# Performance work log

Hardware: AMD Instinct MI355X
Metric: run time of the kernel (lower is better)

The kernel has to match this reference:

```python
import jax, jax.numpy as jnp
import numpy as np

NUM_EXPERTS = 8
EMBED_DIM = 1024
EXPERT_DIM = 2048
TOP_K = 2
B, T = 2, 1024


def setup_inputs() -> dict:
    key = jax.random.key(0)
    ks = jax.random.split(key, 7)
    std = 0.02
    return {
        "x": jax.random.normal(ks[0], (B, T, EMBED_DIM), dtype=jnp.float32),
        "gate_inputs": jax.random.normal(ks[1], (B, T, EMBED_DIM), dtype=jnp.float32),
        "gate_kernel": jax.random.normal(ks[2], (EMBED_DIM, NUM_EXPERTS), dtype=jnp.float32) * std,
        "per_expert_scale": jnp.ones((NUM_EXPERTS,), dtype=jnp.float32),
        "gate_proj_w": jax.random.normal(ks[3], (NUM_EXPERTS, EMBED_DIM, EXPERT_DIM), dtype=jnp.float32) * std,
        "up_proj_w": jax.random.normal(ks[4], (NUM_EXPERTS, EMBED_DIM, EXPERT_DIM), dtype=jnp.float32) * std,
        "down_proj_w": jax.random.normal(ks[5], (NUM_EXPERTS, EXPERT_DIM, EMBED_DIM), dtype=jnp.float32) * std,
    }


def reference(x, gate_inputs, gate_kernel, per_expert_scale,
              gate_proj_w, up_proj_w, down_proj_w):
    Bb, Tt, D = x.shape
    x_flat = x.reshape(Bb * Tt, D)          # [t, e]
    g_flat = gate_inputs.reshape(Bb * Tt, D)

    logits = jnp.dot(g_flat, gate_kernel)   # [t, n]
    topk_logits, topk_idx = jax.lax.top_k(logits, TOP_K)  # [t, k]
    weights = jax.nn.sigmoid(topk_logits)   # [t, k]

    # Dense all-expert projections (as in the original module)
    gate_out = jnp.einsum('te,ned->tnd', x_flat, gate_proj_w)  # [t, n, d]
    up_out = jnp.einsum('te,ned->tnd', x_flat, up_proj_w)
    act = jax.nn.gelu(gate_out) * up_out
    expert_out = jnp.einsum('tnd,nde->tne', act, down_proj_w)  # [t, n, e]
    expert_out = expert_out * per_expert_scale[None, :, None]

    mask = jax.nn.one_hot(topk_idx, NUM_EXPERTS, dtype=expert_out.dtype)  # [t, k, n]
    selected = jnp.einsum('tkn,tne->tke', mask, expert_out)               # [t, k, e]
    out = jnp.einsum('tk,tke->te', weights, selected)                     # [t, e]
    return out.reshape(Bb, Tt, D)
```

## Files before the change

### kernel.cpp

```cpp
#include <hip/hip_runtime.h>
#include <math.h>
#include <stdint.h>

#define NE 8
#define ED 1024
#define FD 2048
#define NTOK 2048
#define BM 128
#define BN 128
#define BK 64

typedef unsigned short u16;
typedef unsigned int u32;
typedef __attribute__((ext_vector_type(4))) float f32x4;
typedef __attribute__((ext_vector_type(8))) short s16x8;
typedef __attribute__((ext_vector_type(4))) unsigned int u32v4;


__device__ __forceinline__ u16 f2bf(float f) {
    u32 u = __builtin_bit_cast(u32, f);
    u32 r = u + 0x7fffu + ((u >> 16) & 1u);
    return (u16)(r >> 16);
}

typedef __attribute__((address_space(1))) const void gvoid_t;
typedef __attribute__((address_space(3))) void lvoid_t;

__device__ __forceinline__ void gload16(const void* g, void* l) {
    __builtin_amdgcn_global_load_lds((gvoid_t*)g, (lvoid_t*)l, 16, 0, 0);
}

#define WS_CNT 0u
#define WS_OFF 64u
#define WS_TOK 256u
#define WS_WT  65792u
#define WS_XB  131328u
#define WS_WG  (8u << 20)
#define WS_WU  41943040u
#define WS_WD  75497472u
#define WS_ACT 109051904u
#define WS_NEED 130023424u


__global__ __launch_bounds__(256) void k_router(
        const float* __restrict__ gin, const float* __restrict__ gk,
        int* __restrict__ cnt, int* __restrict__ tok, float* __restrict__ wl) {
    int lane = threadIdx.x & 63;
    int t = (blockIdx.x * 256 + threadIdx.x) >> 6;
    if (t >= NTOK) return;
    const float* row = gin + (size_t)t * ED;
    float acc[NE];
#pragma unroll
    for (int e = 0; e < NE; e++) acc[e] = 0.f;
    for (int i = lane; i < ED; i += 64) {
        float v = row[i];
        const float* g = gk + i * NE;
#pragma unroll
        for (int e = 0; e < NE; e++) acc[e] = fmaf(v, g[e], acc[e]);
    }
#pragma unroll
    for (int e = 0; e < NE; e++) {
#pragma unroll
        for (int off = 32; off > 0; off >>= 1)
            acc[e] += __shfl_down(acc[e], off, 64);
    }
    if (lane == 0) {
        int b0 = 0; float v0 = acc[0];
#pragma unroll
        for (int e = 1; e < NE; e++) if (acc[e] > v0) { v0 = acc[e]; b0 = e; }
        int b1 = -1; float v1 = -3.4e38f;
#pragma unroll
        for (int e = 0; e < NE; e++) if (e != b0 && acc[e] > v1) { v1 = acc[e]; b1 = e; }
        float w0 = 1.f / (1.f + __expf(-v0));
        float w1 = 1.f / (1.f + __expf(-v1));
        int p0 = atomicAdd(&cnt[b0], 1);
        tok[b0 * NTOK + p0] = t; wl[b0 * NTOK + p0] = w0;
        int p1 = atomicAdd(&cnt[b1], 1);
        tok[b1 * NTOK + p1] = t; wl[b1 * NTOK + p1] = w1;
    }
}

__global__ void k_scan(const int* __restrict__ cnt, int* __restrict__ off) {
    if (threadIdx.x == 0 && blockIdx.x == 0) {
        int a = 0;
#pragma unroll
        for (int e = 0; e < NE; e++) { off[e] = a; a += (cnt[e] + 127) & ~127; }
        off[NE] = a;
    }
}


__global__ __launch_bounds__(256) void k_cvtx(const float4* __restrict__ x, uint2* __restrict__ xb) {
    int i = blockIdx.x * 256 + threadIdx.x;
    float4 v = x[i];
    uint2 o;
    o.x = (u32)f2bf(v.x) | ((u32)f2bf(v.y) << 16);
    o.y = (u32)f2bf(v.z) | ((u32)f2bf(v.w) << 16);
    xb[i] = o;
}


__global__ __launch_bounds__(256) void k_cvtw(
        const float* __restrict__ wgf, const float* __restrict__ wuf, const float* __restrict__ wdf,
        u16* __restrict__ og, u16* __restrict__ ou, u16* __restrict__ od) {
    int b = blockIdx.x;
    const float* src; u16* dst; int NT, KC, ROW;
    if (b < 2048)      { src = wgf; dst = og; NT = 16; KC = 16; ROW = FD; }
    else if (b < 4096) { b -= 2048; src = wuf; dst = ou; NT = 16; KC = 16; ROW = FD; }
    else               { b -= 4096; src = wdf; dst = od; NT = 8;  KC = 32; ROW = ED; }
    int kc = b % KC; int r = b / KC; int nt = r % NT; int e = r / NT;
    const float* base = src + (size_t)e * (size_t)(KC * 64) * ROW + (size_t)kc * 64 * ROW + nt * 128;
    u16* ob = dst + (size_t)b * 8192;

    int tid = threadIdx.x;
    int k0 = (tid & 7) * 8;
    int n0 = tid >> 3;
#pragma unroll
    for (int g4 = 0; g4 < 4; g4++) {
        int n = n0 + 32 * g4;
        const float* p = base + n;
        u32 w[4];
#pragma unroll
        for (int j = 0; j < 4; j++) {
            float a = p[(size_t)(k0 + 2 * j) * ROW];
            float c = p[(size_t)(k0 + 2 * j + 1) * ROW];
            w[j] = (u32)f2bf(a) | ((u32)f2bf(c) << 16);
        }
        *(u32v4*)(ob + (size_t)n * 64 + k0) = (u32v4){w[0], w[1], w[2], w[3]};
    }
}


__global__ __launch_bounds__(256, 2) void k_passA(
        const u16* __restrict__ xb, const u16* __restrict__ wg, const u16* __restrict__ wu,
        const int* __restrict__ cnt, const int* __restrict__ off,
        const int* __restrict__ tok, u16* __restrict__ act) {
    int e = blockIdx.z, mt = blockIdx.y, nt = blockIdx.x;
    int c = cnt[e];
    if (mt * BM >= c) return;
    int rmax = c - mt * BM; if (rmax > BM) rmax = BM;

    __shared__ u16 sA[BM * BK];
    __shared__ u16 sBg[BN * BK];
    __shared__ u16 sBu[BN * BK];

    int tid = threadIdx.x;
    int lane = tid & 63, wv = tid >> 6;
    int wm = wv >> 1, wn = wv & 1;
    int col = lane & 15, quad = lane >> 4;

    f32x4 zero = {0.f, 0.f, 0.f, 0.f};
    f32x4 ag[4][4], au[4][4];
#pragma unroll
    for (int i = 0; i < 4; i++)
#pragma unroll
        for (int j = 0; j < 4; j++) { ag[i][j] = zero; au[i][j] = zero; }

    int am = tid >> 1, ah = tid & 1;
    int ridx = mt * BM + am; if (ridx > c - 1) ridx = c - 1;
    int trow = tok[e * NTOK + ridx];
    const u16* asrc = xb + (size_t)trow * ED + ah * 32;
    u16* adst = sA + am * BK + ah * 32;

    const u16* gg = wg + ((size_t)(e * 16 + nt) * 16) * 8192;
    const u16* gu = wu + ((size_t)(e * 16 + nt) * 16) * 8192;
    const u16* bsrc0 = (wv < 2 ? gg : gu);
    int bhalf = (wv & 1) * 4096;
    u16* bdst = (wv < 2 ? sBg : sBu) + bhalf;

    for (int kc = 0; kc < 16; kc++) {
        __syncthreads();
        const u16* bs = bsrc0 + (size_t)kc * 8192 + bhalf + lane * 8;
#pragma unroll
        for (int i = 0; i < 8; i++)
            gload16(bs + i * 512, bdst + i * 512);
        const u16* as = asrc + kc * 64;
        u32v4 v0 = *(const u32v4*)(as);
        u32v4 v1 = *(const u32v4*)(as + 8);
        u32v4 v2 = *(const u32v4*)(as + 16);
        u32v4 v3 = *(const u32v4*)(as + 24);
        *(u32v4*)(adst) = v0;
        *(u32v4*)(adst + 8) = v1;
        *(u32v4*)(adst + 16) = v2;
        *(u32v4*)(adst + 24) = v3;
        __syncthreads();
#pragma unroll
        for (int st = 0; st < 2; st++) {
            s16x8 af[4];
#pragma unroll
            for (int mf = 0; mf < 4; mf++)
                af[mf] = *(const s16x8*)(sA + (wm * 64 + mf * 16 + col) * BK + st * 32 + quad * 8);
#pragma unroll
            for (int nf = 0; nf < 4; nf++) {
                int brow = (wn * 64 + nf * 16 + col) * BK + st * 32 + quad * 8;
                s16x8 bg = *(const s16x8*)(sBg + brow);
                s16x8 bu = *(const s16x8*)(sBu + brow);
#pragma unroll
                for (int mf = 0; mf < 4; mf++) {
                    ag[mf][nf] = __builtin_amdgcn_mfma_f32_16x16x32_bf16(af[mf], bg, ag[mf][nf], 0, 0, 0);
                    au[mf][nf] = __builtin_amdgcn_mfma_f32_16x16x32_bf16(af[mf], bu, au[mf][nf], 0, 0, 0);
                }
            }
        }
    }

    int tile = (off[e] >> 7) + mt;
    u16* ab = act + (size_t)tile * (32 * 8192);
#pragma unroll
    for (int mf = 0; mf < 4; mf++) {
#pragma unroll
        for (int reg = 0; reg < 4; reg++) {
            int m = wm * 64 + mf * 16 + quad * 4 + reg;
            if (m < rmax) {
#pragma unroll
                for (int nf = 0; nf < 4; nf++) {
                    float gv = ag[mf][nf][reg];
                    float uv = au[mf][nf][reg];
                    float z = 0.7978845608028654f * (gv + 0.044715f * gv * gv * gv);
                    float ez = __expf(-2.f * fabsf(z));
                    float th = (1.f - ez) / (1.f + ez);
                    th = (z < 0.f) ? -th : th;
                    float a = 0.5f * gv * (1.f + th) * uv;
                    int ng = nt * 128 + wn * 64 + nf * 16 + col;
                    ab[((size_t)(ng >> 6) * 128 + m) * 64 + (ng & 63)] = f2bf(a);
                }
            }
        }
    }
}


__global__ __launch_bounds__(256, 3) void k_passB(
        const u16* __restrict__ act, const u16* __restrict__ wd,
        const int* __restrict__ cnt, const int* __restrict__ off,
        const int* __restrict__ tok, const float* __restrict__ wl,
        const float* __restrict__ scale, float* __restrict__ out) {
    int e = blockIdx.z, mt = blockIdx.y, nt = blockIdx.x;
    int c = cnt[e];
    if (mt * BM >= c) return;
    int rmax = c - mt * BM; if (rmax > BM) rmax = BM;

    __shared__ u16 sA[BM * BK];
    __shared__ u16 sB[BN * BK];

    int tid = threadIdx.x;
    int lane = tid & 63, wv = tid >> 6;
    int wm = wv >> 1, wn = wv & 1;
    int col = lane & 15, quad = lane >> 4;

    f32x4 zero = {0.f, 0.f, 0.f, 0.f};
    f32x4 acc[4][4];
#pragma unroll
    for (int i = 0; i < 4; i++)
#pragma unroll
        for (int j = 0; j < 4; j++) acc[i][j] = zero;

    int tile = (off[e] >> 7) + mt;
    const u16* ga = act + (size_t)tile * (32 * 8192);
    const u16* gb = wd + ((size_t)(e * 8 + nt) * 32) * 8192;
    const u16* src0 = (wv < 2 ? ga : gb);
    int shalf = (wv & 1) * 4096;
    u16* dst0 = (wv < 2 ? sA : sB) + shalf;

    for (int kc = 0; kc < 32; kc++) {
        __syncthreads();
        const u16* s = src0 + (size_t)kc * 8192 + shalf + lane * 8;
#pragma unroll
        for (int i = 0; i < 8; i++)
            gload16(s + i * 512, dst0 + i * 512);
        __syncthreads();
#pragma unroll
        for (int st = 0; st < 2; st++) {
            s16x8 af[4];
#pragma unroll
            for (int mf = 0; mf < 4; mf++)
                af[mf] = *(const s16x8*)(sA + (wm * 64 + mf * 16 + col) * BK + st * 32 + quad * 8);
#pragma unroll
            for (int nf = 0; nf < 4; nf++) {
                int brow = (wn * 64 + nf * 16 + col) * BK + st * 32 + quad * 8;
                s16x8 bf = *(const s16x8*)(sB + brow);
#pragma unroll
                for (int mf = 0; mf < 4; mf++)
                    acc[mf][nf] = __builtin_amdgcn_mfma_f32_16x16x32_bf16(af[mf], bf, acc[mf][nf], 0, 0, 0);
            }
        }
    }

    float sc = scale[e];
    int lbase = e * NTOK + mt * BM;
#pragma unroll
    for (int mf = 0; mf < 4; mf++) {
#pragma unroll
        for (int reg = 0; reg < 4; reg++) {
            int m = wm * 64 + mf * 16 + quad * 4 + reg;
            if (m < rmax) {
                int t = tok[lbase + m];
                float w = wl[lbase + m] * sc;
                float* orow = out + (size_t)t * ED + nt * 128 + wn * 64 + col;
#pragma unroll
                for (int nf = 0; nf < 4; nf++)
                    atomicAdd(orow + nf * 16, acc[mf][nf][reg] * w);
            }
        }
    }
}


extern "C" void kernel_launch(void* const* d_in, const int* in_sizes, int n_in,
                              void* d_out, int out_size, void* d_ws, size_t ws_size,
                              hipStream_t stream) {
    const float* x   = (const float*)d_in[0];
    const float* gin = (const float*)d_in[1];
    const float* gk  = (const float*)d_in[2];
    const float* sc  = (const float*)d_in[3];
    const float* wgf = (const float*)d_in[4];
    const float* wuf = (const float*)d_in[5];
    const float* wdf = (const float*)d_in[6];
    float* out = (float*)d_out;

    if (ws_size < (size_t)WS_NEED) {
        hipMemsetAsync(d_out, 0, (size_t)out_size * sizeof(float), stream);
        return;
    }

    char* ws = (char*)d_ws;
    int*   cnt = (int*)(ws + WS_CNT);
    int*   off = (int*)(ws + WS_OFF);
    int*   tok = (int*)(ws + WS_TOK);
    float* wl  = (float*)(ws + WS_WT);
    u16*   xb  = (u16*)(ws + WS_XB);
    u16*   og  = (u16*)(ws + WS_WG);
    u16*   ou  = (u16*)(ws + WS_WU);
    u16*   od  = (u16*)(ws + WS_WD);
    u16*   act = (u16*)(ws + WS_ACT);

    hipMemsetAsync(cnt, 0, 64, stream);
    hipMemsetAsync(d_out, 0, (size_t)out_size * sizeof(float), stream);

    k_router<<<dim3(512), dim3(256), 0, stream>>>(gin, gk, cnt, tok, wl);
    k_scan<<<dim3(1), dim3(64), 0, stream>>>(cnt, off);
    k_cvtx<<<dim3(2048), dim3(256), 0, stream>>>((const float4*)x, (uint2*)xb);
    k_cvtw<<<dim3(6144), dim3(256), 0, stream>>>(wgf, wuf, wdf, og, ou, od);
    k_passA<<<dim3(16, 16, NE), dim3(256), 0, stream>>>(xb, og, ou, cnt, off, tok, act);
    k_passB<<<dim3(8, 16, NE), dim3(256), 0, stream>>>(act, od, cnt, off, tok, wl, sc, out);
}
```

Before: 452.4 us.

## XOR-swizzle bf16 tile layouts to avoid LDS bank conflicts; transpose weights via LDS

Stores weight, activation and x tiles with an XOR swizzle of the 8-element k-groups by row index. The MFMA fragment reads from LDS then spread across banks instead of many rows hitting the same banks. The weight conversion kernel now reads rows with coalesced float4 loads into a padded shared buffer and transposes from there, instead of doing strided global reads. Every producer and consumer must agree on the swizzle; a mismatch would silently corrupt results.

```diff
diff --git a/kernel.cpp b/kernel.cpp
--- a/kernel.cpp
+++ b/kernel.cpp
@@ -29,6 +29,7 @@
 __device__ __forceinline__ void gload16(const void* g, void* l) {
     __builtin_amdgcn_global_load_lds((gvoid_t*)g, (lvoid_t*)l, 16, 0, 0);
 }
+
 
 #define WS_CNT 0u
 #define WS_OFF 64u
@@ -110,23 +111,38 @@
     else               { b -= 4096; src = wdf; dst = od; NT = 8;  KC = 32; ROW = ED; }
     int kc = b % KC; int r = b / KC; int nt = r % NT; int e = r / NT;
     const float* base = src + (size_t)e * (size_t)(KC * 64) * ROW + (size_t)kc * 64 * ROW + nt * 128;
-    u16* ob = dst + (size_t)b * 8192;
-
+    u16* ob = dst + (size_t)(blockIdx.x < 2048 ? blockIdx.x :
+                             (blockIdx.x < 4096 ? blockIdx.x - 2048 : blockIdx.x - 4096)) * 8192;
+
+    __shared__ float sl[64 * 129];
     int tid = threadIdx.x;
-    int k0 = (tid & 7) * 8;
-    int n0 = tid >> 3;
-#pragma unroll
-    for (int g4 = 0; g4 < 4; g4++) {
-        int n = n0 + 32 * g4;
-        const float* p = base + n;
+
+    {
+        int k = tid >> 2, q = tid & 3;
+        const float* rp = base + (size_t)k * ROW;
+        float* lp = sl + k * 129;
+#pragma unroll
+        for (int j = 0; j < 8; j++) {
+            int n0 = (q + 4 * j) * 4;
+            float4 v = *(const float4*)(rp + n0);
+            lp[n0] = v.x; lp[n0 + 1] = v.y; lp[n0 + 2] = v.z; lp[n0 + 3] = v.w;
+        }
+    }
+    __syncthreads();
+
+#pragma unroll
+    for (int jg = 0; jg < 4; jg++) {
+        int v = tid + 256 * jg;
+        int n = v >> 3, p = v & 7;
+        int k0 = (p ^ (n & 7)) * 8;
         u32 w[4];
 #pragma unroll
-        for (int j = 0; j < 4; j++) {
-            float a = p[(size_t)(k0 + 2 * j) * ROW];
-            float c = p[(size_t)(k0 + 2 * j + 1) * ROW];
-            w[j] = (u32)f2bf(a) | ((u32)f2bf(c) << 16);
-        }
-        *(u32v4*)(ob + (size_t)n * 64 + k0) = (u32v4){w[0], w[1], w[2], w[3]};
+        for (int u = 0; u < 4; u++) {
+            float a = sl[(k0 + 2 * u) * 129 + n];
+            float c = sl[(k0 + 2 * u + 1) * 129 + n];
+            w[u] = (u32)f2bf(a) | ((u32)f2bf(c) << 16);
+        }
+        *(u32v4*)(ob + (size_t)n * 64 + p * 8) = (u32v4){w[0], w[1], w[2], w[3]};
     }
 }
 
@@ -148,6 +164,7 @@
     int lane = tid & 63, wv = tid >> 6;
     int wm = wv >> 1, wn = wv & 1;
     int col = lane & 15, quad = lane >> 4;
+    int swz = col & 7;
 
     f32x4 zero = {0.f, 0.f, 0.f, 0.f};
     f32x4 ag[4][4], au[4][4];
@@ -160,7 +177,7 @@
     int ridx = mt * BM + am; if (ridx > c - 1) ridx = c - 1;
     int trow = tok[e * NTOK + ridx];
     const u16* asrc = xb + (size_t)trow * ED + ah * 32;
-    u16* adst = sA + am * BK + ah * 32;
+    u16* adst = sA + am * BK;
 
     const u16* gg = wg + ((size_t)(e * 16 + nt) * 16) * 8192;
     const u16* gu = wu + ((size_t)(e * 16 + nt) * 16) * 8192;
@@ -175,24 +192,22 @@
         for (int i = 0; i < 8; i++)
             gload16(bs + i * 512, bdst + i * 512);
         const u16* as = asrc + kc * 64;
-        u32v4 v0 = *(const u32v4*)(as);
-        u32v4 v1 = *(const u32v4*)(as + 8);
-        u32v4 v2 = *(const u32v4*)(as + 16);
-        u32v4 v3 = *(const u32v4*)(as + 24);
-        *(u32v4*)(adst) = v0;
-        *(u32v4*)(adst + 8) = v1;
-        *(u32v4*)(adst + 16) = v2;
-        *(u32v4*)(adst + 24) = v3;
+#pragma unroll
+        for (int j = 0; j < 4; j++) {
+            int pg = (ah * 4 + j) ^ (am & 7);
+            *(u32v4*)(adst + pg * 8) = *(const u32v4*)(as + j * 8);
+        }
         __syncthreads();
 #pragma unroll
         for (int st = 0; st < 2; st++) {
+            int poff = ((st * 4 + quad) ^ swz) * 8;
             s16x8 af[4];
 #pragma unroll
             for (int mf = 0; mf < 4; mf++)
-                af[mf] = *(const s16x8*)(sA + (wm * 64 + mf * 16 + col) * BK + st * 32 + quad * 8);
+                af[mf] = *(const s16x8*)(sA + (wm * 64 + mf * 16 + col) * BK + poff);
 #pragma unroll
             for (int nf = 0; nf < 4; nf++) {
-                int brow = (wn * 64 + nf * 16 + col) * BK + st * 32 + quad * 8;
+                int brow = (wn * 64 + nf * 16 + col) * BK + poff;
                 s16x8 bg = *(const s16x8*)(sBg + brow);
                 s16x8 bu = *(const s16x8*)(sBu + brow);
 #pragma unroll
@@ -222,7 +237,8 @@
                     th = (z < 0.f) ? -th : th;
                     float a = 0.5f * gv * (1.f + th) * uv;
                     int ng = nt * 128 + wn * 64 + nf * 16 + col;
-                    ab[((size_t)(ng >> 6) * 128 + m) * 64 + (ng & 63)] = f2bf(a);
+                    int pos = ((((ng >> 3) & 7) ^ (m & 7)) * 8) | (ng & 7);
+                    ab[(size_t)(ng >> 6) * 8192 + (size_t)m * 64 + pos] = f2bf(a);
                 }
             }
         }
@@ -247,6 +263,7 @@
     int lane = tid & 63, wv = tid >> 6;
     int wm = wv >> 1, wn = wv & 1;
     int col = lane & 15, quad = lane >> 4;
+    int swz = col & 7;
 
     f32x4 zero = {0.f, 0.f, 0.f, 0.f};
     f32x4 acc[4][4];
@@ -271,13 +288,14 @@
         __syncthreads();
 #pragma unroll
         for (int st = 0; st < 2; st++) {
+            int poff = ((st * 4 + quad) ^ swz) * 8;
             s16x8 af[4];
 #pragma unroll
             for (int mf = 0; mf < 4; mf++)
-                af[mf] = *(const s16x8*)(sA + (wm * 64 + mf * 16 + col) * BK + st * 32 + quad * 8);
+                af[mf] = *(const s16x8*)(sA + (wm * 64 + mf * 16 + col) * BK + poff);
 #pragma unroll
             for (int nf = 0; nf < 4; nf++) {
-                int brow = (wn * 64 + nf * 16 + col) * BK + st * 32 + quad * 8;
+                int brow = (wn * 64 + nf * 16 + col) * BK + poff;
                 s16x8 bf = *(const s16x8*)(sB + brow);
 #pragma unroll
                 for (int mf = 0; mf < 4; mf++)
```

Result: faster. 405.4 us (-10.4%).
